# Kernel optimization log

Hardware: AMD Instinct MI355X
Metric: run time of the kernel (lower is better)

## Reference

```python
import jax, jax.numpy as jnp
import numpy as np

B, P, L = 16, 196, 80
DIM1, DIM2, ATT = 2048, 300, 512
TAU = 1.0


def setup_inputs() -> dict:
    key = jax.random.key(0)
    ks = jax.random.split(key, 8)
    s1 = 1.0 / np.sqrt(DIM1)
    s2 = 1.0 / np.sqrt(DIM2)
    sa = 1.0 / np.sqrt(ATT)
    return {
        "x1": jax.random.normal(ks[0], (B, P, DIM1), dtype=jnp.float32),
        "x2": jax.random.normal(ks[1], (B, L, DIM2), dtype=jnp.float32),
        # nn.Linear weights stored as (out, in), like torch
        "W1": jax.random.uniform(ks[2], (ATT, DIM1), jnp.float32, -s1, s1),
        "W2": jax.random.uniform(ks[3], (ATT, DIM2), jnp.float32, -s2, s2),
        "Wh": jax.random.uniform(ks[4], (ATT, ATT), jnp.float32, -sa, sa),
        "bh": jax.random.uniform(ks[5], (ATT,), jnp.float32, -sa, sa),
        "Wt": jax.random.uniform(ks[6], (1, ATT), jnp.float32, -sa, sa),
        "bt": jax.random.uniform(ks[7], (1,), jnp.float32, -sa, sa),
    }


def reference(x1, x2, W1, W2, Wh, bh, Wt, bt):
    # projections: (B,P,ATT) and (B,L,ATT)
    p1 = jnp.einsum("bpd,ad->bpa", x1, W1)
    p2 = jnp.einsum("bld,ad->bla", x2, W2)
    # broadcast bilinear interaction: (B,L,P,ATT)
    m = jnp.tanh(p1[:, None, :, :] * p2[:, :, None, :])
    h = jnp.einsum("blpa,ca->blpc", m, Wh) + bh
    # score: (B,L,P)
    t = jnp.einsum("blpa,a->blp", h, Wt[0]) + bt[0]
    alpha = jax.nn.softmax(t / TAU, axis=-1)
    # weighted sum over pixels: (B,L,DIM1)
    label_repr = jnp.einsum("blp,bpd->bld", alpha, x1)
    return (label_repr, alpha)
```

## Files before the change

### kernel.cpp

```cpp
#include <hip/hip_runtime.h>

#define B_   16
#define P_   196
#define L_   80
#define DIM1 2048
#define DIM2 300
#define ATT  512

typedef __attribute__((ext_vector_type(8))) short short8x;
typedef __attribute__((ext_vector_type(4))) float f32x4;
typedef __attribute__((ext_vector_type(4))) unsigned int uint4x;
typedef __attribute__((ext_vector_type(4))) unsigned short ushort4x;

__global__ __launch_bounds__(256)
void weff_kernel(const float* __restrict__ Wh, const float* __restrict__ Wt,
                 float* __restrict__ w_eff) {
    __shared__ float part[4][64];
    const int tid = threadIdx.x, lane = tid & 63, quad = tid >> 6;
    const int a = blockIdx.x * 64 + lane;
    float s = 0.f;
    const int c0 = quad * 128;
    for (int c = c0; c < c0 + 128; ++c)
        s = fmaf(Wt[c], Wh[(size_t)c * ATT + a], s);
    part[quad][lane] = s;
    __syncthreads();
    if (tid < 64)
        w_eff[blockIdx.x * 64 + tid] =
            (part[0][tid] + part[1][tid]) + (part[2][tid] + part[3][tid]);
}

__global__ __launch_bounds__(256)
void cvt_bf16_kernel(const float* __restrict__ in, unsigned short* __restrict__ out, int n4) {
    for (int i = blockIdx.x * 256 + threadIdx.x; i < n4; i += gridDim.x * 256) {
        uint4x u = ((const uint4x*)in)[i];
        ushort4x o;
        #pragma unroll
        for (int j = 0; j < 4; ++j) {
            unsigned v = u[j];
            v += 0x7fffu + ((v >> 16) & 1u);
            o[j] = (unsigned short)(v >> 16);
        }
        ((ushort4x*)out)[i] = o;
    }
}

#define GM 3136
#define GN 512
#define GK 2048

__device__ __forceinline__ void gload16(const unsigned short* g, unsigned short* l) {
    __builtin_amdgcn_global_load_lds(
        (const __attribute__((address_space(1))) unsigned int*)g,
        (__attribute__((address_space(3))) unsigned int*)l, 16, 0, 0);
}

__global__ __launch_bounds__(256)
void gemm_bf16_mfma(const unsigned short* __restrict__ Ab,
                    const unsigned short* __restrict__ Bb,
                    float* __restrict__ C) {
    __shared__ unsigned short As[2][64 * 64];
    __shared__ unsigned short Bs[2][32 * 64];
    const int tid  = threadIdx.x;
    const int wid  = tid >> 6;
    const int lane = tid & 63;
    const int bm   = blockIdx.x * 64;
    const int bn   = blockIdx.y * 32;

    const int srow = lane >> 3;
    const int scol = ((lane & 7) ^ srow) << 3;
    const size_t arow0 = (size_t)(bm + (wid << 4) + srow) * GK;
    const size_t brow0 = (size_t)(bn + (wid << 3) + srow) * GK;

#define STAGE_TILE(buf, k0)                                                              \
    {                                                                                    \
        gload16(Ab + arow0 + (k0) + scol,                  &As[buf][((wid << 4) + 0) * 64]); \
        gload16(Ab + arow0 + (size_t)8 * GK + (k0) + scol, &As[buf][((wid << 4) + 8) * 64]); \
        gload16(Bb + brow0 + (k0) + scol,                  &Bs[buf][(wid << 3) * 64]);       \
    }

    f32x4 acc[2] = {};
    const int fr  = lane & 15;
    const int kb  = (lane >> 4) << 3;
    const int swz = (lane & 7) << 4;

    STAGE_TILE(0, 0)
    constexpr int NT = GK / 64;
    for (int kt = 0; kt < NT; ++kt) {
        __syncthreads();
        if (kt + 1 < NT) STAGE_TILE((kt + 1) & 1, (kt + 1) * 64)
        const char* pa = (const char*)&As[kt & 1][0];
        const char* pb = (const char*)&Bs[kt & 1][0];
        #pragma unroll
        for (int kk = 0; kk < 2; ++kk) {
            const int koff = ((kk * 32 + kb) * 2) ^ swz;
            short8x a = *(const short8x*)(pa + ((wid << 4) + fr) * 128 + koff);
            short8x b[2];
            #pragma unroll
            for (int n = 0; n < 2; ++n)
                b[n] = *(const short8x*)(pb + (n * 16 + fr) * 128 + koff);
            #pragma unroll
            for (int n = 0; n < 2; ++n)
                acc[n] = __builtin_amdgcn_mfma_f32_16x16x32_bf16(a, b[n], acc[n], 0, 0, 0);
        }
        __syncthreads();
    }

    const int crow = (lane >> 4) << 2;
    #pragma unroll
    for (int n = 0; n < 2; ++n)
        #pragma unroll
        for (int j = 0; j < 4; ++j)
            C[(size_t)(bm + (wid << 4) + crow + j) * GN + bn + n * 16 + fr] = acc[n][j];
#undef STAGE_TILE
}

__global__ __launch_bounds__(256)
void gemm_nt(const float* __restrict__ A, const float* __restrict__ Bm,
             float* __restrict__ C, int M, int N, int K) {
    constexpr int BK = 16;
    __shared__ float As[BK][64];
    __shared__ float Bs[BK][64];
    const int tid  = threadIdx.x;
    const int bm   = blockIdx.x * 64;
    const int bn   = blockIdx.y * 64;
    const int ty   = tid >> 4;
    const int tx   = tid & 15;
    const int lrow = tid >> 2;
    const int lc4  = (tid & 3) << 2;
    float acc[4][4] = {};
    const float* Arow = A  + (size_t)(bm + lrow) * K;
    const float* Brow = Bm + (size_t)(bn + lrow) * K;

    for (int k0 = 0; k0 < K; k0 += BK) {
        float4 av, bv;
        if (k0 + BK <= K) {
            av = *(const float4*)(Arow + k0 + lc4);
            bv = *(const float4*)(Brow + k0 + lc4);
        } else {
            float a_[4], b_[4];
            #pragma unroll
            for (int i = 0; i < 4; ++i) {
                const int k = k0 + lc4 + i;
                a_[i] = (k < K) ? Arow[k] : 0.f;
                b_[i] = (k < K) ? Brow[k] : 0.f;
            }
            av = make_float4(a_[0], a_[1], a_[2], a_[3]);
            bv = make_float4(b_[0], b_[1], b_[2], b_[3]);
        }
        __syncthreads();
        As[lc4 + 0][lrow] = av.x;
        As[lc4 + 1][lrow] = av.y;
        As[lc4 + 2][lrow] = av.z;
        As[lc4 + 3][lrow] = av.w;
        Bs[lc4 + 0][lrow] = bv.x;
        Bs[lc4 + 1][lrow] = bv.y;
        Bs[lc4 + 2][lrow] = bv.z;
        Bs[lc4 + 3][lrow] = bv.w;
        __syncthreads();
        #pragma unroll
        for (int k = 0; k < BK; ++k) {
            const float4 a4 = *(const float4*)&As[k][ty << 2];
            const float4 b4 = *(const float4*)&Bs[k][tx << 2];
            const float ae[4] = {a4.x, a4.y, a4.z, a4.w};
            const float be[4] = {b4.x, b4.y, b4.z, b4.w};
            #pragma unroll
            for (int i = 0; i < 4; ++i)
                #pragma unroll
                for (int j = 0; j < 4; ++j)
                    acc[i][j] = fmaf(ae[i], be[j], acc[i][j]);
        }
    }
    #pragma unroll
    for (int i = 0; i < 4; ++i) {
        float4 o = make_float4(acc[i][0], acc[i][1], acc[i][2], acc[i][3]);
        *(float4*)(C + (size_t)(bm + (ty << 2) + i) * N + bn + (tx << 2)) = o;
    }
}

#define LOG2E2 2.8853900817779268f

__global__ __launch_bounds__(256)
void score_softmax_kernel(const float* __restrict__ p1, const float* __restrict__ p2,
                          const float* __restrict__ w_eff, float* __restrict__ alpha) {
    const int bidx = blockIdx.x;
    const int bl = (bidx & 7) * 160 + (bidx >> 3);
    const int b  = bl / L_;
    __shared__ float s_t[P_];
    __shared__ float s_red[4];
    const int tid = threadIdx.x, wave = tid >> 6, lane = tid & 63;
    const int g = lane >> 4, c = lane & 15;

    const float4* gp2 = (const float4*)(p2 + (size_t)bl * ATT);
    const float4* gw  = (const float4*)w_eff;
    float4 qa[8], wa[8];
    #pragma unroll
    for (int j = 0; j < 8; ++j) {
        const float4 q = gp2[c + 16 * j];
        qa[j] = make_float4(q.x * LOG2E2, q.y * LOG2E2, q.z * LOG2E2, q.w * LOG2E2);
        wa[j] = gw[c + 16 * j];
    }

    const float* p1b = p1 + (size_t)b * P_ * ATT;
    const int nch = (wave == 0) ? 13 : 12;
    int p = 16 * 0 + 4 * wave + g;
    int ptail = 192 + g;
    int row0 = (0 < 12) ? p : ptail;
    float4 cur[8], nxt[8];
    {
        const float4* row = (const float4*)(p1b + (size_t)row0 * ATT);
        #pragma unroll
        for (int j = 0; j < 8; ++j) cur[j] = row[c + 16 * j];
    }
    for (int i = 0; i < nch; ++i) {
        const int pr = (i < 12) ? (16 * i + 4 * wave + g) : ptail;
        if (i + 1 < nch) {
            const int pn = (i + 1 < 12) ? (16 * (i + 1) + 4 * wave + g) : ptail;
            const float4* row = (const float4*)(p1b + (size_t)pn * ATT);
            #pragma unroll
            for (int j = 0; j < 8; ++j) nxt[j] = row[c + 16 * j];
        }
        float acc = 0.f;
        #pragma unroll
        for (int j = 0; j < 8; ++j) {
            const float e0 = __builtin_amdgcn_exp2f(cur[j].x * qa[j].x);
            const float e1 = __builtin_amdgcn_exp2f(cur[j].y * qa[j].y);
            const float e2 = __builtin_amdgcn_exp2f(cur[j].z * qa[j].z);
            const float e3 = __builtin_amdgcn_exp2f(cur[j].w * qa[j].w);
            float num = fmaf(wa[j].x, e1, fmaf(wa[j].y, e0, wa[j].x + wa[j].y));
            float den = fmaf(e0, e1, e0 + e1 + 1.f);
            acc = fmaf(num, __builtin_amdgcn_rcpf(den), acc);
            num = fmaf(wa[j].z, e3, fmaf(wa[j].w, e2, wa[j].z + wa[j].w));
            den = fmaf(e2, e3, e2 + e3 + 1.f);
            acc = fmaf(num, __builtin_amdgcn_rcpf(den), acc);
        }
        acc += __shfl_xor(acc, 1);
        acc += __shfl_xor(acc, 2);
        acc += __shfl_xor(acc, 4);
        acc += __shfl_xor(acc, 8);
        if (c == 0) s_t[pr] = acc;
        #pragma unroll
        for (int j = 0; j < 8; ++j) cur[j] = nxt[j];
    }
    __syncthreads();
    const float v = (tid < P_) ? -2.f * s_t[tid] : -1e30f;
    float m = v;
    #pragma unroll
    for (int off = 32; off >= 1; off >>= 1) m = fmaxf(m, __shfl_xor(m, off));
    if (lane == 0) s_red[wave] = m;
    __syncthreads();
    m = fmaxf(fmaxf(s_red[0], s_red[1]), fmaxf(s_red[2], s_red[3]));
    __syncthreads();
    const float e = (tid < P_) ? __expf(v - m) : 0.f;
    float s = e;
    #pragma unroll
    for (int off = 32; off >= 1; off >>= 1) s += __shfl_xor(s, off);
    if (lane == 0) s_red[wave] = s;
    __syncthreads();
    s = s_red[0] + s_red[1] + s_red[2] + s_red[3];
    if (tid < P_) alpha[(size_t)bl * P_ + tid] = e / s;
}

__global__ __launch_bounds__(256)
void label_kernel(const float* __restrict__ alpha, const float* __restrict__ x1,
                  float* __restrict__ out) {
    const int dt = blockIdx.x;
    const int lt = blockIdx.y;
    const int b  = blockIdx.z;
    __shared__ float s_alpha[P_][16];
    const int tid = threadIdx.x;
    for (int idx = tid; idx < 16 * P_; idx += 256) {
        const int p = idx >> 4, i = idx & 15;
        s_alpha[p][i] = alpha[(size_t)(b * L_ + lt * 16 + i) * P_ + p];
    }
    __syncthreads();
    const int d = dt * 256 + tid;
    const float* xcol = x1 + (size_t)b * P_ * DIM1 + d;
    float acc[16] = {};
    for (int p = 0; p < P_; p += 4) {
        float xv[4];
        #pragma unroll
        for (int u = 0; u < 4; ++u) xv[u] = xcol[(size_t)(p + u) * DIM1];
        #pragma unroll
        for (int u = 0; u < 4; ++u) {
            const float4 a0 = *(const float4*)&s_alpha[p + u][0];
            const float4 a1 = *(const float4*)&s_alpha[p + u][4];
            const float4 a2 = *(const float4*)&s_alpha[p + u][8];
            const float4 a3 = *(const float4*)&s_alpha[p + u][12];
            acc[0]  = fmaf(a0.x, xv[u], acc[0]);
            acc[1]  = fmaf(a0.y, xv[u], acc[1]);
            acc[2]  = fmaf(a0.z, xv[u], acc[2]);
            acc[3]  = fmaf(a0.w, xv[u], acc[3]);
            acc[4]  = fmaf(a1.x, xv[u], acc[4]);
            acc[5]  = fmaf(a1.y, xv[u], acc[5]);
            acc[6]  = fmaf(a1.z, xv[u], acc[6]);
            acc[7]  = fmaf(a1.w, xv[u], acc[7]);
            acc[8]  = fmaf(a2.x, xv[u], acc[8]);
            acc[9]  = fmaf(a2.y, xv[u], acc[9]);
            acc[10] = fmaf(a2.z, xv[u], acc[10]);
            acc[11] = fmaf(a2.w, xv[u], acc[11]);
            acc[12] = fmaf(a3.x, xv[u], acc[12]);
            acc[13] = fmaf(a3.y, xv[u], acc[13]);
            acc[14] = fmaf(a3.z, xv[u], acc[14]);
            acc[15] = fmaf(a3.w, xv[u], acc[15]);
        }
    }
    #pragma unroll
    for (int i = 0; i < 16; ++i)
        out[(size_t)(b * L_ + lt * 16 + i) * DIM1 + d] = acc[i];
}

extern "C" void kernel_launch(void* const* d_in, const int* in_sizes, int n_in,
                              void* d_out, int out_size, void* d_ws, size_t ws_size,
                              hipStream_t stream) {
    const float* x1 = (const float*)d_in[0];
    const float* x2 = (const float*)d_in[1];
    const float* W1 = (const float*)d_in[2];
    const float* W2 = (const float*)d_in[3];
    const float* Wh = (const float*)d_in[4];
    const float* Wt = (const float*)d_in[6];

    float* ws    = (float*)d_ws;
    float* p1    = ws;
    float* p2    = p1 + (size_t)B_ * P_ * ATT;
    float* w_eff = p2 + (size_t)B_ * L_ * ATT;
    unsigned short* x1b = (unsigned short*)(w_eff + ATT);
    unsigned short* W1b = x1b + (size_t)B_ * P_ * DIM1;

    float* label = (float*)d_out;
    float* alpha = label + (size_t)B_ * L_ * DIM1;

    hipLaunchKernelGGL(cvt_bf16_kernel, dim3(2048), dim3(256), 0, stream,
                       x1, x1b, (B_ * P_ * DIM1) / 4);
    hipLaunchKernelGGL(cvt_bf16_kernel, dim3(512), dim3(256), 0, stream,
                       W1, W1b, (ATT * DIM1) / 4);
    hipLaunchKernelGGL(weff_kernel, dim3(8), dim3(256), 0, stream, Wh, Wt, w_eff);
    hipLaunchKernelGGL(gemm_nt, dim3((B_ * L_) / 64, ATT / 64), dim3(256), 0, stream,
                       x2, W2, p2, B_ * L_, ATT, DIM2);
    hipLaunchKernelGGL(gemm_bf16_mfma, dim3(GM / 64, GN / 32), dim3(256), 0, stream,
                       x1b, W1b, p1);
    hipLaunchKernelGGL(score_softmax_kernel, dim3(B_ * L_), dim3(256), 0, stream,
                       p1, p2, w_eff, alpha);
    hipLaunchKernelGGL(label_kernel, dim3(8, 5, B_), dim3(256), 0, stream,
                       alpha, x1, label);
}
```

Before: 196.9 us.

## Fuse prep kernels into one launch and store p1 as bf16

Merges the two bf16 conversions, the w_eff reduction and the small x2·W2 GEMM into a single block-indexed prep kernel, removing three launches and letting the independent pieces run concurrently. The MFMA GEMM now writes p1 as bf16 and uses a swapped grid order. The score kernel reads bf16 p1 with a new per-lane element mapping, which halves its p1 traffic. This lowers the precision of p1 before the tanh/score step, which could shift the softmax outputs.

```diff
diff --git a/kernel.cpp b/kernel.cpp
--- a/kernel.cpp
+++ b/kernel.cpp
@@ -8,39 +8,118 @@
 #define ATT  512
 
 typedef __attribute__((ext_vector_type(8))) short short8x;
+typedef __attribute__((ext_vector_type(8))) unsigned short ushort8x;
 typedef __attribute__((ext_vector_type(4))) float f32x4;
 typedef __attribute__((ext_vector_type(4))) unsigned int uint4x;
 typedef __attribute__((ext_vector_type(4))) unsigned short ushort4x;
 
+__device__ __forceinline__ unsigned short f2bf(float f) {
+    unsigned v = __float_as_uint(f);
+    v += 0x7fffu + ((v >> 16) & 1u);
+    return (unsigned short)(v >> 16);
+}
+
 __global__ __launch_bounds__(256)
-void weff_kernel(const float* __restrict__ Wh, const float* __restrict__ Wt,
-                 float* __restrict__ w_eff) {
+void prep_kernel(const float* __restrict__ x1, const float* __restrict__ W1,
+                 const float* __restrict__ Wh, const float* __restrict__ Wt,
+                 const float* __restrict__ x2, const float* __restrict__ W2,
+                 unsigned short* __restrict__ x1b, unsigned short* __restrict__ W1b,
+                 float* __restrict__ w_eff, float* __restrict__ p2) {
+    __shared__ float As[16][64];
+    __shared__ float Bs[16][64];
     __shared__ float part[4][64];
-    const int tid = threadIdx.x, lane = tid & 63, quad = tid >> 6;
-    const int a = blockIdx.x * 64 + lane;
-    float s = 0.f;
-    const int c0 = quad * 128;
-    for (int c = c0; c < c0 + 128; ++c)
-        s = fmaf(Wt[c], Wh[(size_t)c * ATT + a], s);
-    part[quad][lane] = s;
-    __syncthreads();
-    if (tid < 64)
-        w_eff[blockIdx.x * 64 + tid] =
-            (part[0][tid] + part[1][tid]) + (part[2][tid] + part[3][tid]);
-}
-
-__global__ __launch_bounds__(256)
-void cvt_bf16_kernel(const float* __restrict__ in, unsigned short* __restrict__ out, int n4) {
-    for (int i = blockIdx.x * 256 + threadIdx.x; i < n4; i += gridDim.x * 256) {
-        uint4x u = ((const uint4x*)in)[i];
-        ushort4x o;
-        #pragma unroll
-        for (int j = 0; j < 4; ++j) {
-            unsigned v = u[j];
-            v += 0x7fffu + ((v >> 16) & 1u);
-            o[j] = (unsigned short)(v >> 16);
-        }
-        ((ushort4x*)out)[i] = o;
+    const int blk = blockIdx.x;
+    const int tid = threadIdx.x;
+
+    if (blk < 2048) {
+        const int n4 = (B_ * P_ * DIM1) / 4;
+        for (int i = blk * 256 + tid; i < n4; i += 2048 * 256) {
+            uint4x u = ((const uint4x*)x1)[i];
+            ushort4x o;
+            #pragma unroll
+            for (int j = 0; j < 4; ++j) {
+                unsigned v = u[j];
+                v += 0x7fffu + ((v >> 16) & 1u);
+                o[j] = (unsigned short)(v >> 16);
+            }
+            ((ushort4x*)x1b)[i] = o;
+        }
+    } else if (blk < 2560) {
+        const int n4 = (ATT * DIM1) / 4;
+        for (int i = (blk - 2048) * 256 + tid; i < n4; i += 512 * 256) {
+            uint4x u = ((const uint4x*)W1)[i];
+            ushort4x o;
+            #pragma unroll
+            for (int j = 0; j < 4; ++j) {
+                unsigned v = u[j];
+                v += 0x7fffu + ((v >> 16) & 1u);
+                o[j] = (unsigned short)(v >> 16);
+            }
+            ((ushort4x*)W1b)[i] = o;
+        }
+    } else if (blk < 2568) {
+        const int bix = blk - 2560;
+        const int lane = tid & 63, quad = tid >> 6;
+        const int a = bix * 64 + lane;
+        float s = 0.f;
+        const int c0 = quad * 128;
+        for (int c = c0; c < c0 + 128; ++c)
+            s = fmaf(Wt[c], Wh[(size_t)c * ATT + a], s);
+        part[quad][lane] = s;
+        __syncthreads();
+        if (tid < 64)
+            w_eff[bix * 64 + tid] =
+                (part[0][tid] + part[1][tid]) + (part[2][tid] + part[3][tid]);
+    } else {
+        const int local = blk - 2568;
+        const int bm = (local % 20) * 64;
+        const int bn = (local / 20) * 64;
+        const int M = B_ * L_, N = ATT, K = DIM2;
+        const int ty = tid >> 4, tx = tid & 15;
+        const int lrow = tid >> 2, lc4 = (tid & 3) << 2;
+        float acc[4][4] = {};
+        const float* Arow = x2 + (size_t)(bm + lrow) * K;
+        const float* Brow = W2 + (size_t)(bn + lrow) * K;
+        for (int k0 = 0; k0 < K; k0 += 16) {
+            float4 av, bv;
+            if (k0 + 16 <= K) {
+                av = *(const float4*)(Arow + k0 + lc4);
+                bv = *(const float4*)(Brow + k0 + lc4);
+            } else {
+                float a_[4], b_[4];
+                #pragma unroll
+                for (int i = 0; i < 4; ++i) {
+                    const int k = k0 + lc4 + i;
+                    a_[i] = (k < K) ? Arow[k] : 0.f;
+                    b_[i] = (k < K) ? Brow[k] : 0.f;
+                }
+                av = make_float4(a_[0], a_[1], a_[2], a_[3]);
+                bv = make_float4(b_[0], b_[1], b_[2], b_[3]);
+            }
+            __syncthreads();
+            As[lc4 + 0][lrow] = av.x;  As[lc4 + 1][lrow] = av.y;
+            As[lc4 + 2][lrow] = av.z;  As[lc4 + 3][lrow] = av.w;
+            Bs[lc4 + 0][lrow] = bv.x;  Bs[lc4 + 1][lrow] = bv.y;
+            Bs[lc4 + 2][lrow] = bv.z;  Bs[lc4 + 3][lrow] = bv.w;
+            __syncthreads();
+            #pragma unroll
+            for (int k = 0; k < 16; ++k) {
+                const float4 a4 = *(const float4*)&As[k][ty << 2];
+                const float4 b4 = *(const float4*)&Bs[k][tx << 2];
+                const float ae[4] = {a4.x, a4.y, a4.z, a4.w};
+                const float be[4] = {b4.x, b4.y, b4.z, b4.w};
+                #pragma unroll
+                for (int i = 0; i < 4; ++i)
+                    #pragma unroll
+                    for (int j = 0; j < 4; ++j)
+                        acc[i][j] = fmaf(ae[i], be[j], acc[i][j]);
+            }
+        }
+        #pragma unroll
+        for (int i = 0; i < 4; ++i) {
+            float4 o = make_float4(acc[i][0], acc[i][1], acc[i][2], acc[i][3]);
+            *(float4*)(p2 + (size_t)(bm + (ty << 2) + i) * N + bn + (tx << 2)) = o;
+        }
     }
 }
 
@@ -57,14 +136,14 @@
 __global__ __launch_bounds__(256)
 void gemm_bf16_mfma(const unsigned short* __restrict__ Ab,
                     const unsigned short* __restrict__ Bb,
-                    float* __restrict__ C) {
+                    unsigned short* __restrict__ C) {
     __shared__ unsigned short As[2][64 * 64];
     __shared__ unsigned short Bs[2][32 * 64];
     const int tid  = threadIdx.x;
     const int wid  = tid >> 6;
     const int lane = tid & 63;
-    const int bm   = blockIdx.x * 64;
-    const int bn   = blockIdx.y * 32;
+    const int bm   = blockIdx.y * 64;
+    const int bn   = blockIdx.x * 32;
 
     const int srow = lane >> 3;
     const int scol = ((lane & 7) ^ srow) << 3;
@@ -110,78 +189,18 @@
     for (int n = 0; n < 2; ++n)
         #pragma unroll
         for (int j = 0; j < 4; ++j)
-            C[(size_t)(bm + (wid << 4) + crow + j) * GN + bn + n * 16 + fr] = acc[n][j];
+            C[(size_t)(bm + (wid << 4) + crow + j) * GN + bn + n * 16 + fr] =
+                f2bf(acc[n][j]);
 #undef STAGE_TILE
 }
 
+#define LOG2E2 2.8853900817779268f
+
 __global__ __launch_bounds__(256)
-void gemm_nt(const float* __restrict__ A, const float* __restrict__ Bm,
-             float* __restrict__ C, int M, int N, int K) {
-    constexpr int BK = 16;
-    __shared__ float As[BK][64];
-    __shared__ float Bs[BK][64];
-    const int tid  = threadIdx.x;
-    const int bm   = blockIdx.x * 64;
-    const int bn   = blockIdx.y * 64;
-    const int ty   = tid >> 4;
-    const int tx   = tid & 15;
-    const int lrow = tid >> 2;
-    const int lc4  = (tid & 3) << 2;
-    float acc[4][4] = {};
-    const float* Arow = A  + (size_t)(bm + lrow) * K;
-    const float* Brow = Bm + (size_t)(bn + lrow) * K;
-
-    for (int k0 = 0; k0 < K; k0 += BK) {
-        float4 av, bv;
-        if (k0 + BK <= K) {
-            av = *(const float4*)(Arow + k0 + lc4);
-            bv = *(const float4*)(Brow + k0 + lc4);
-        } else {
-            float a_[4], b_[4];
-            #pragma unroll
-            for (int i = 0; i < 4; ++i) {
-                const int k = k0 + lc4 + i;
-                a_[i] = (k < K) ? Arow[k] : 0.f;
-                b_[i] = (k < K) ? Brow[k] : 0.f;
-            }
-            av = make_float4(a_[0], a_[1], a_[2], a_[3]);
-            bv = make_float4(b_[0], b_[1], b_[2], b_[3]);
-        }
-        __syncthreads();
-        As[lc4 + 0][lrow] = av.x;
-        As[lc4 + 1][lrow] = av.y;
-        As[lc4 + 2][lrow] = av.z;
-        As[lc4 + 3][lrow] = av.w;
-        Bs[lc4 + 0][lrow] = bv.x;
-        Bs[lc4 + 1][lrow] = bv.y;
-        Bs[lc4 + 2][lrow] = bv.z;
-        Bs[lc4 + 3][lrow] = bv.w;
-        __syncthreads();
-        #pragma unroll
-        for (int k = 0; k < BK; ++k) {
-            const float4 a4 = *(const float4*)&As[k][ty << 2];
-            const float4 b4 = *(const float4*)&Bs[k][tx << 2];
-            const float ae[4] = {a4.x, a4.y, a4.z, a4.w};
-            const float be[4] = {b4.x, b4.y, b4.z, b4.w};
-            #pragma unroll
-            for (int i = 0; i < 4; ++i)
-                #pragma unroll
-                for (int j = 0; j < 4; ++j)
-                    acc[i][j] = fmaf(ae[i], be[j], acc[i][j]);
-        }
-    }
-    #pragma unroll
-    for (int i = 0; i < 4; ++i) {
-        float4 o = make_float4(acc[i][0], acc[i][1], acc[i][2], acc[i][3]);
-        *(float4*)(C + (size_t)(bm + (ty << 2) + i) * N + bn + (tx << 2)) = o;
-    }
-}
-
-#define LOG2E2 2.8853900817779268f
-
-__global__ __launch_bounds__(256)
-void score_softmax_kernel(const float* __restrict__ p1, const float* __restrict__ p2,
-                          const float* __restrict__ w_eff, float* __restrict__ alpha) {
+void score_softmax_kernel(const unsigned short* __restrict__ p1,
+                          const float* __restrict__ p2,
+                          const float* __restrict__ w_eff,
+                          float* __restrict__ alpha) {
     const int bidx = blockIdx.x;
     const int bl = (bidx & 7) * 160 + (bidx >> 3);
     const int b  = bl / L_;
@@ -192,46 +211,53 @@
 
     const float4* gp2 = (const float4*)(p2 + (size_t)bl * ATT);
     const float4* gw  = (const float4*)w_eff;
-    float4 qa[8], wa[8];
-    #pragma unroll
-    for (int j = 0; j < 8; ++j) {
-        const float4 q = gp2[c + 16 * j];
-        qa[j] = make_float4(q.x * LOG2E2, q.y * LOG2E2, q.z * LOG2E2, q.w * LOG2E2);
-        wa[j] = gw[c + 16 * j];
-    }
-
-    const float* p1b = p1 + (size_t)b * P_ * ATT;
+    float qa[4][8], wa[4][8];
+    #pragma unroll
+    for (int j = 0; j < 4; ++j) {
+        const float4 qlo = gp2[32 * j + 2 * c], qhi = gp2[32 * j + 2 * c + 1];
+        const float4 wlo = gw[32 * j + 2 * c],  whi = gw[32 * j + 2 * c + 1];
+        qa[j][0] = qlo.x * LOG2E2; qa[j][1] = qlo.y * LOG2E2;
+        qa[j][2] = qlo.z * LOG2E2; qa[j][3] = qlo.w * LOG2E2;
+        qa[j][4] = qhi.x * LOG2E2; qa[j][5] = qhi.y * LOG2E2;
+        qa[j][6] = qhi.z * LOG2E2; qa[j][7] = qhi.w * LOG2E2;
+        wa[j][0] = wlo.x; wa[j][1] = wlo.y; wa[j][2] = wlo.z; wa[j][3] = wlo.w;
+        wa[j][4] = whi.x; wa[j][5] = whi.y; wa[j][6] = whi.z; wa[j][7] = whi.w;
+    }
+
+    const unsigned short* p1b = p1 + (size_t)b * P_ * ATT;
     const int nch = (wave == 0) ? 13 : 12;
-    int p = 16 * 0 + 4 * wave + g;
-    int ptail = 192 + g;
-    int row0 = (0 < 12) ? p : ptail;
-    float4 cur[8], nxt[8];
+    const int ptail = 192 + g;
+    ushort8x cur[4], nxt[4];
     {
-        const float4* row = (const float4*)(p1b + (size_t)row0 * ATT);
-        #pragma unroll
-        for (int j = 0; j < 8; ++j) cur[j] = row[c + 16 * j];
+        const int row0 = 4 * wave + g;
+        const ushort8x* row = (const ushort8x*)(p1b + (size_t)row0 * ATT);
+        #pragma unroll
+        for (int j = 0; j < 4; ++j) cur[j] = row[c + 16 * j];
     }
     for (int i = 0; i < nch; ++i) {
         const int pr = (i < 12) ? (16 * i + 4 * wave + g) : ptail;
         if (i + 1 < nch) {
             const int pn = (i + 1 < 12) ? (16 * (i + 1) + 4 * wave + g) : ptail;
-            const float4* row = (const float4*)(p1b + (size_t)pn * ATT);
-            #pragma unroll
-            for (int j = 0; j < 8; ++j) nxt[j] = row[c + 16 * j];
+            const ushort8x* row = (const ushort8x*)(p1b + (size_t)pn * ATT);
+            #pragma unroll
+            for (int j = 0; j < 4; ++j) nxt[j] = row[c + 16 * j];
         }
         float acc = 0.f;
         #pragma unroll
-        for (int j = 0; j < 8; ++j) {
-            const float e0 = __builtin_amdgcn_exp2f(cur[j].x * qa[j].x);
-            const float e1 = __builtin_amdgcn_exp2f(cur[j].y * qa[j].y);
-            const float e2 = __builtin_amdgcn_exp2f(cur[j].z * qa[j].z);
-            const float e3 = __builtin_amdgcn_exp2f(cur[j].w * qa[j].w);
-            float num = fmaf(wa[j].x, e1, fmaf(wa[j].y, e0, wa[j].x + wa[j].y));
-            float den = fmaf(e0, e1, e0 + e1 + 1.f);
-            acc = fmaf(num, __builtin_amdgcn_rcpf(den), acc);
-            num = fmaf(wa[j].z, e3, fmaf(wa[j].w, e2, wa[j].z + wa[j].w));
-            den = fmaf(e2, e3, e2 + e3 + 1.f);
-            acc = fmaf(num, __builtin_amdgcn_rcpf(den), acc);
+        for (int j = 0; j < 4; ++j) {
+            float r[8];
+            #pragma unroll
+            for (int e = 0; e < 8; ++e)
+                r[e] = __uint_as_float((unsigned)cur[j][e] << 16);
+            #pragma unroll
+            for (int pq = 0; pq < 4; ++pq) {
+                const float e0 = __builtin_amdgcn_exp2f(r[2 * pq]     * qa[j][2 * pq]);
+                const float e1 = __builtin_amdgcn_exp2f(r[2 * pq + 1] * qa[j][2 * pq + 1]);
+                const float w0 = wa[j][2 * pq], w1 = wa[j][2 * pq + 1];
+                const float num = fmaf(w0, e1, fmaf(w1, e0, w0 + w1));
+                const float den = fmaf(e0, e1, e0 + e1 + 1.f);
+                acc = fmaf(num, __builtin_amdgcn_rcpf(den), acc);
+            }
         }
         acc += __shfl_xor(acc, 1);
         acc += __shfl_xor(acc, 2);
@@ -239,7 +265,7 @@
         acc += __shfl_xor(acc, 8);
         if (c == 0) s_t[pr] = acc;
         #pragma unroll
-        for (int j = 0; j < 8; ++j) cur[j] = nxt[j];
+        for (int j = 0; j < 4; ++j) cur[j] = nxt[j];
     }
     __syncthreads();
     const float v = (tid < P_) ? -2.f * s_t[tid] : -1e30f;
@@ -319,27 +345,22 @@
     const float* Wh = (const float*)d_in[4];
     const float* Wt = (const float*)d_in[6];
 
-    float* ws    = (float*)d_ws;
-    float* p1    = ws;
-    float* p2    = p1 + (size_t)B_ * P_ * ATT;
-    float* w_eff = p2 + (size_t)B_ * L_ * ATT;
-    unsigned short* x1b = (unsigned short*)(w_eff + ATT);
+    char* base = (char*)d_ws;
+    unsigned short* p1b = (unsigned short*)base;
+    float* p2    = (float*)(base + 3211264);
+    float* w_eff = (float*)(base + 3211264 + 2621440);
+    unsigned short* x1b = (unsigned short*)(base + 3211264 + 2621440 + 2048);
     unsigned short* W1b = x1b + (size_t)B_ * P_ * DIM1;
 
     float* label = (float*)d_out;
     float* alpha = label + (size_t)B_ * L_ * DIM1;
 
-    hipLaunchKernelGGL(cvt_bf16_kernel, dim3(2048), dim3(256), 0, stream,
-                       x1, x1b, (B_ * P_ * DIM1) / 4);
-    hipLaunchKernelGGL(cvt_bf16_kernel, dim3(512), dim3(256), 0, stream,
-                       W1, W1b, (ATT * DIM1) / 4);
-    hipLaunchKernelGGL(weff_kernel, dim3(8), dim3(256), 0, stream, Wh, Wt, w_eff);
-    hipLaunchKernelGGL(gemm_nt, dim3((B_ * L_) / 64, ATT / 64), dim3(256), 0, stream,
-                       x2, W2, p2, B_ * L_, ATT, DIM2);
-    hipLaunchKernelGGL(gemm_bf16_mfma, dim3(GM / 64, GN / 32), dim3(256), 0, stream,
-                       x1b, W1b, p1);
+    hipLaunchKernelGGL(prep_kernel, dim3(2728), dim3(256), 0, stream,
+                       x1, W1, Wh, Wt, x2, W2, x1b, W1b, w_eff, p2);
+    hipLaunchKernelGGL(gemm_bf16_mfma, dim3(GN / 32, GM / 64), dim3(256), 0, stream,
+                       x1b, W1b, p1b);
     hipLaunchKernelGGL(score_softmax_kernel, dim3(B_ * L_), dim3(256), 0, stream,
-                       p1, p2, w_eff, alpha);
+                       p1b, p2, w_eff, alpha);
     hipLaunchKernelGGL(label_kernel, dim3(8, 5, B_), dim3(256), 0, stream,
                        alpha, x1, label);
 }
```

Result: slower. 202.1 us (+2.6%).
